# Kernel optimization log

Hardware: AMD Instinct MI355X
Metric: run time of the kernel (lower is better)

The kernel has to match this reference:

```python
import jax, jax.numpy as jnp
import numpy as np

# sym8 decomposition low-pass filter (pywt convention, 16 taps)
SYM8_DEC_LO = np.array([
    -0.0033824159510061256, -0.0005421323317911481, 0.03169508781149298,
    0.007607487324917605, -0.1432942383508097, -0.061273359067658524,
    0.4813596512583722, 0.7771857517005235, 0.3644418948353314,
    -0.05194583810770904, -0.027219029917056003, 0.049137179673607506,
    0.003808752013890615, -0.01495225833704823, -0.0003029205147213668,
    0.0018899503327594609], dtype=np.float64)

MAX_LEV = 8
POWER = 2.0
EPS = 1e-12


def _filters():
    dec_lo = jnp.asarray(SYM8_DEC_LO, dtype=jnp.float32)
    n = dec_lo.shape[0]
    alt = jnp.where(jnp.arange(n) % 2 == 0, 1.0, -1.0).astype(jnp.float32)
    dec_hi = alt * dec_lo[::-1]  # quadrature mirror filter
    # conv_general_dilated is cross-correlation (like torch conv1d in ptwt),
    # so flip the decomposition filters.
    return jnp.stack([dec_lo[::-1], dec_hi[::-1]])[:, None, :]  # [2,1,F] OIW


def _dwt_step(x, filt):
    # x: [N, L] -> [2N, L_out]; per node the (approx, detail) pair is interleaved,
    # which yields pywt 'natural' packet order after repeated application.
    F = filt.shape[-1]
    L = x.shape[1]
    padl = (2 * F - 3) // 2            # ptwt _fwt_pad, reflect mode
    padr = padl + (L % 2)              # extra right pad for odd lengths
    xp = jnp.pad(x, ((0, 0), (padl, padr)), mode='reflect')
    y = jax.lax.conv_general_dilated(
        xp[:, None, :], filt, window_strides=(2,), padding='VALID')  # [N,2,L']
    return y.reshape(-1, y.shape[-1])


def reference(pt_data):
    B = pt_data.shape[0]
    filt = _filters()
    x = pt_data
    for _ in range(MAX_LEV):           # fixed, small tree depth (8 levels)
        x = _dwt_step(x, filt)
    wp = x.reshape(B, 2 ** MAX_LEV, -1)         # [B, 256, L_final] natural order
    wp_log = jnp.log(jnp.abs(wp) ** POWER + EPS)
    # torch: stack(dim=-1) -> [B, L, P]; unsqueeze(1); permute(0,1,3,2) -> [B,1,P,L]
    return wp_log[:, None]             # [B, 1, 256, L_final]


def setup_inputs() -> dict:
    key = jax.random.key(0)
    pt_data = jax.random.normal(key, (128, 65536), dtype=jnp.float32)
    return {"pt_data": pt_data}
```

## Files before the change

kernel.cpp:

```cpp
#include <hip/hip_runtime.h>


#define BT 512

__device__ __constant__ float FL[16] = {
     0.0018899503327594609f, -0.0003029205147213668f, -0.01495225833704823f,
     0.003808752013890615f,   0.049137179673607506f,  -0.027219029917056003f,
    -0.05194583810770904f,    0.3644418948353314f,     0.7771857517005235f,
     0.4813596512583722f,    -0.061273359067658524f,  -0.1432942383508097f,
     0.007607487324917605f,   0.03169508781149298f,   -0.0005421323317911481f,
    -0.0033824159510061256f
};

__device__ __constant__ float FH[16] = {
     0.0033824159510061256f, -0.0005421323317911481f, -0.03169508781149298f,
     0.007607487324917605f,   0.1432942383508097f,    -0.061273359067658524f,
    -0.4813596512583722f,     0.7771857517005235f,    -0.3644418948353314f,
    -0.05194583810770904f,    0.027219029917056003f,   0.049137179673607506f,
    -0.003808752013890615f,  -0.01495225833704823f,    0.0003029205147213668f,
     0.0018899503327594609f
};

__device__ __constant__ float FLE[8] = {
     0.0018899503327594609f, -0.01495225833704823f,  0.049137179673607506f,
    -0.05194583810770904f,   0.7771857517005235f,   -0.061273359067658524f,
     0.007607487324917605f, -0.0005421323317911481f };
__device__ __constant__ float FLO[8] = {
    -0.0003029205147213668f, 0.003808752013890615f, -0.027219029917056003f,
     0.3644418948353314f,    0.4813596512583722f,   -0.1432942383508097f,
     0.03169508781149298f,  -0.0033824159510061256f };
__device__ __constant__ float FHE[8] = {
     0.0033824159510061256f, -0.03169508781149298f,  0.1432942383508097f,
    -0.4813596512583722f,   -0.3644418948353314f,    0.027219029917056003f,
    -0.003808752013890615f,  0.0003029205147213668f };
__device__ __constant__ float FHO[8] = {
    -0.0005421323317911481f, 0.007607487324917605f, -0.061273359067658524f,
     0.7771857517005235f,   -0.05194583810770904f,   0.049137179673607506f,
    -0.01495225833704823f,   0.0018899503327594609f };

__device__ __forceinline__ int reflect(int q, int L) {
    q = (q < 0) ? -q : q;
    return (q >= L) ? (2 * L - 2 - q) : q;
}

__device__ __forceinline__ void load20(const float* __restrict__ lds, int base,
                                       float w[20]) {
#pragma unroll
    for (int k = 0; k < 5; ++k) {
        const float4 v = *reinterpret_cast<const float4*>(&lds[base + 4 * k]);
        w[4 * k] = v.x; w[4 * k + 1] = v.y; w[4 * k + 2] = v.z; w[4 * k + 3] = v.w;
    }
}

__device__ __forceinline__ void conv2(const float w[20], float& lo0, float& hi0,
                                      float& lo1, float& hi1) {
    lo0 = hi0 = lo1 = hi1 = 0.f;
#pragma unroll
    for (int t = 0; t < 16; ++t) {
        const float cl = FL[t], ch = FH[t];
        lo0 = fmaf(w[t], cl, lo0);
        hi0 = fmaf(w[t], ch, hi0);
        lo1 = fmaf(w[t + 2], cl, lo1);
        hi1 = fmaf(w[t + 2], ch, hi1);
    }
}

template <int Pin, int Wout, int Sin, int Sout, int Lc>
__device__ __forceinline__ void f03_stage(const float* __restrict__ in,
                                          float* __restrict__ out, int o_lo) {
    constexpr int GPS = Wout / 2;
    for (int g = threadIdx.x; g < Pin * GPS; g += BT) {
        const int r = g / GPS;
        const int u = g - r * GPS;
        const int s0 = 2 * u;
        const int q0 = o_lo + s0;
        const float* pin = in + r * Sin;
        float lo0, hi0, lo1, hi1;
        if (q0 >= 0 && q0 + 2 <= Lc) {
            float w[20];
            load20(pin, 4 * u, w);
            conv2(w, lo0, hi0, lo1, hi1);
        } else {
#pragma unroll
            for (int e = 0; e < 2; ++e) {
                const int jr = reflect(q0 + e, Lc);
                const int rb = 2 * (jr - o_lo);
                float l = 0.f, h = 0.f;
#pragma unroll
                for (int t = 0; t < 16; ++t) {
                    const float v = pin[rb + t];
                    l = fmaf(v, FL[t], l);
                    h = fmaf(v, FH[t], h);
                }
                if (e == 0) { lo0 = l; hi0 = h; } else { lo1 = l; hi1 = h; }
            }
        }
        *reinterpret_cast<float2*>(&out[(2 * r) * Sout + s0])     = make_float2(lo0, lo1);
        *reinterpret_cast<float2*>(&out[(2 * r + 1) * Sout + s0]) = make_float2(hi0, hi1);
    }
}

__global__ __launch_bounds__(BT, 8) void dwt_f03(
    const float* __restrict__ x, float* __restrict__ y) {
    constexpr int M  = 258;
    constexpr int WX = 4338, SX = 4340;
    constexpr int W0 = 2162, S0 = 2164;
    constexpr int W1 = 1074, S1 = 1076;
    constexpr int W2 = 530,  S2 = 532;
    __shared__ __align__(16) float bufA[4340];
    __shared__ __align__(16) float bufB[4328];

    const int seg = blockIdx.x;
    const int n   = blockIdx.y;
    const int b0  = M * seg;
    const int a2  = 2 * b0 - 14;
    const int c1  = 4 * b0 - 42;
    const int a0  = 8 * b0 - 98;
    const int px0 = 16 * b0 - 210;
    const float* row = x + (size_t)n * 65536;

    if (px0 >= 0 && px0 + WX <= 65536) {
        const float2* rp = reinterpret_cast<const float2*>(row + px0);
        for (int h = threadIdx.x; h < WX / 2; h += BT)
            *reinterpret_cast<float2*>(&bufA[2 * h]) = rp[h];
    } else {
        for (int p = threadIdx.x; p < WX; p += BT)
            bufA[p] = row[reflect(px0 + p, 65536)];
    }
    __syncthreads();

    f03_stage<1, W0, SX, S0, 32775>(bufA, bufB, a0);
    __syncthreads();
    f03_stage<2, W1, S0, S1, 16395>(bufB, bufA, c1);
    __syncthreads();
    f03_stage<4, W2, S1, S2, 8205>(bufA, bufB, a2);
    __syncthreads();

    {
        constexpr int GPS = M / 2;
        float* yg = y + (size_t)(16 * n) * 4112;
        for (int g = threadIdx.x; g < 8 * GPS; g += BT) {
            const int r  = g / GPS;
            const int u  = g - r * GPS;
            const int j0 = b0 + 2 * u;
            if (j0 >= 4110) continue;
            float w[20];
            load20(bufB + r * S2, 4 * u, w);
            float lo0, hi0, lo1, hi1;
            conv2(w, lo0, hi0, lo1, hi1);
            float* y0 = yg + (size_t)(2 * r) * 4112 + j0;
            float* y1 = y0 + 4112;
            if (j0 + 1 < 4110) {
                *reinterpret_cast<float2*>(y0) = make_float2(lo0, lo1);
                *reinterpret_cast<float2*>(y1) = make_float2(hi0, hi1);
            } else {
                y0[0] = lo0; y1[0] = hi0;
            }
        }
    }
}

__device__ __forceinline__ void eo_put(float* __restrict__ E, float* __restrict__ O,
                                       int q, float v) {
    ((q & 1) ? O : E)[8 + (q >> 1)] = v;
}

__device__ __forceinline__ void read12(const float* __restrict__ b, int w0,
                                       float* __restrict__ r) {
#pragma unroll
    for (int k = 0; k < 3; ++k) {
        const float4 v = *reinterpret_cast<const float4*>(&b[w0 + 4 * k]);
        r[4 * k] = v.x; r[4 * k + 1] = v.y; r[4 * k + 2] = v.z; r[4 * k + 3] = v.w;
    }
}

template <int OFF>
__device__ __forceinline__ void conv4eo(const float e[12], const float o[12],
                                        float lo[4], float hi[4]) {
#pragma unroll
    for (int d = 0; d < 4; ++d) { lo[d] = 0.f; hi[d] = 0.f; }
#pragma unroll
    for (int s = 0; s < 8; ++s) {
        const float fle = FLE[s], flo = FLO[s], fhe = FHE[s], fho = FHO[s];
#pragma unroll
        for (int d = 0; d < 4; ++d) {
            const float ev = e[OFF + d + s], ov = o[OFF + d + s];
            lo[d] = fmaf(ev, fle, lo[d]);
            lo[d] = fmaf(ov, flo, lo[d]);
            hi[d] = fmaf(ev, fhe, hi[d]);
            hi[d] = fmaf(ov, fho, hi[d]);
        }
    }
}

template <int Ls, int P, int Sin, int Sout, bool LOG>
__device__ __forceinline__ void stage_eo(const float* __restrict__ inb,
                                         float* __restrict__ outb,
                                         float* __restrict__ outg) {
    constexpr int H    = Ls / 2;
    constexpr int LOUT = H + 7;
    constexpr int GPS  = (LOUT + 3) / 4;
    constexpr int SEi  = Sin / 2;
    constexpr int SEo  = Sout / 2;
    for (int g = threadIdx.x; g < P * GPS; g += BT) {
        const int p  = g / GPS;
        const int u  = g - p * GPS;
        const int j0 = 4 * u;
        const float* Ei = inb + p * Sin;
        const float* Oi = Ei + SEi;
        float e[12], o[12];
        read12(Ei, 4 * u, e);
        read12(Oi, 4 * u, o);
        float lo[4], hi[4];
        conv4eo<1>(e, o, lo, hi);
        if (LOG) {
            float r0[4], r1[4];
#pragma unroll
            for (int d = 0; d < 4; ++d) {
                r0[d] = __logf(fmaf(lo[d], lo[d], 1e-12f));
                r1[d] = __logf(fmaf(hi[d], hi[d], 1e-12f));
            }
            float* y0 = outg + (2 * p) * 270 + j0;
            float* y1 = y0 + 270;
            if (j0 + 3 < 270) {
                *reinterpret_cast<float2*>(y0)     = make_float2(r0[0], r0[1]);
                *reinterpret_cast<float2*>(y0 + 2) = make_float2(r0[2], r0[3]);
                *reinterpret_cast<float2*>(y1)     = make_float2(r1[0], r1[1]);
                *reinterpret_cast<float2*>(y1 + 2) = make_float2(r1[2], r1[3]);
            } else {
                *reinterpret_cast<float2*>(y0) = make_float2(r0[0], r0[1]);
                *reinterpret_cast<float2*>(y1) = make_float2(r1[0], r1[1]);
            }
        } else {
            float* El = outb + (2 * p) * Sout;
            float* Ol = El + SEo;
            float* Eh = outb + (2 * p + 1) * Sout;
            float* Oh = Eh + SEo;
            if (j0 + 3 < LOUT) {
                *reinterpret_cast<float2*>(&El[8 + 2 * u]) = make_float2(lo[0], lo[2]);
                *reinterpret_cast<float2*>(&Ol[8 + 2 * u]) = make_float2(lo[1], lo[3]);
                *reinterpret_cast<float2*>(&Eh[8 + 2 * u]) = make_float2(hi[0], hi[2]);
                *reinterpret_cast<float2*>(&Oh[8 + 2 * u]) = make_float2(hi[1], hi[3]);
            } else {
#pragma unroll
                for (int d = 0; d < 4; ++d)
                    if (j0 + d < LOUT) {
                        eo_put(El, Ol, j0 + d, lo[d]);
                        eo_put(Eh, Oh, j0 + d, hi[d]);
                    }
            }
            if (j0 <= 14 || j0 >= LOUT - 18) {
#pragma unroll
                for (int d = 0; d < 4; ++d) {
                    const int j = j0 + d;
                    if (j >= 1 && j <= 14) {
                        eo_put(El, Ol, -j, lo[d]);
                        eo_put(Eh, Oh, -j, hi[d]);
                    }
                    if (j >= LOUT - 15 && j <= LOUT - 2) {
                        eo_put(El, Ol, 2 * LOUT - 2 - j, lo[d]);
                        eo_put(Eh, Oh, 2 * LOUT - 2 - j, hi[d]);
                    }
                }
            }
        }
    }
}

__global__ __launch_bounds__(BT, 8) void dwt_quad_eo(
    const float* __restrict__ x, float* __restrict__ y) {
    __shared__ __align__(16) float bufA[4320];
    __shared__ __align__(16) float bufB[4544];

    const int m = blockIdx.x;
    const float* row = x + (size_t)m * 4112;
    float* Ex = bufA;
    float* Ox = bufA + 2076;
    for (int i = threadIdx.x; i < 2055; i += BT) {
        const float2 v = reinterpret_cast<const float2*>(row)[i];
        Ex[8 + i] = v.x;
        Ox[8 + i] = v.y;
        if (i >= 1 && i <= 7)       eo_put(Ex, Ox, -2 * i, v.x);
        if (i <= 6)                 eo_put(Ex, Ox, -(2 * i + 1), v.y);
        if (i >= 2048)              eo_put(Ex, Ox, 8218 - 2 * i, v.x);
        if (i >= 2047 && i <= 2053) eo_put(Ex, Ox, 8217 - 2 * i, v.y);
    }
    __syncthreads();
    stage_eo<4110, 1, 4152, 2104, false>(bufA, bufB, nullptr);
    __syncthreads();
    stage_eo<2062, 2, 2104, 1080, false>(bufB, bufA, nullptr);
    __syncthreads();
    stage_eo<1038, 4, 1080, 568, false>(bufA, bufB, nullptr);
    __syncthreads();
    stage_eo<526, 8, 568, 0, true>(bufB, nullptr, y + (size_t)m * 4320);
}

extern "C" void kernel_launch(void* const* d_in, const int* in_sizes, int n_in,
                              void* d_out, int out_size, void* d_ws, size_t ws_size,
                              hipStream_t stream) {
    const float* in = (const float*)d_in[0];
    float* out = (float*)d_out;
    float* wsB = (float*)d_ws;
    (void)ws_size; (void)out_size; (void)n_in; (void)in_sizes;

    { dim3 g(16, 128); dwt_f03<<<g, BT, 0, stream>>>(in, wsB); }
    dwt_quad_eo<<<2048, BT, 0, stream>>>(wsB, out);
}
```

Baseline: 74.02 us.

## Write intermediate in even/odd padded layout and load rows via direct global-to-LDS

The first kernel now writes its level-4 output straight into the padded even/odd split layout (including reflected halos) that the second kernel consumes, using a row stride of 4160. The second kernel can then copy each row into LDS with 16-byte direct global-to-LDS loads instead of deinterleaving and writing halos itself. Interior segments of the first kernel also use 4-byte global_load_lds for the input window. The aim is to cut VGPR round-trips and scatter work in the loads, at the cost of scattered strided global stores in the first kernel's epilogue and a slightly larger LDS buffer. The workspace layout changes, and the last 16-byte chunk reads a little past each logical row into padding.

```diff
diff --git a/kernel.cpp b/kernel.cpp
--- a/kernel.cpp
+++ b/kernel.cpp
@@ -11,7 +11,6 @@
      0.007607487324917605f,   0.03169508781149298f,   -0.0005421323317911481f,
     -0.0033824159510061256f
 };
-
 __device__ __constant__ float FH[16] = {
      0.0033824159510061256f, -0.0005421323317911481f, -0.03169508781149298f,
      0.007607487324917605f,   0.1432942383508097f,    -0.061273359067658524f,
@@ -20,7 +19,6 @@
     -0.003808752013890615f,  -0.01495225833704823f,    0.0003029205147213668f,
      0.0018899503327594609f
 };
-
 __device__ __constant__ float FLE[8] = {
      0.0018899503327594609f, -0.01495225833704823f,  0.049137179673607506f,
     -0.05194583810770904f,   0.7771857517005235f,   -0.061273359067658524f,
@@ -43,6 +41,17 @@
     return (q >= L) ? (2 * L - 2 - q) : q;
 }
 
+__device__ __forceinline__ void gload_lds16(const float* g, float* l) {
+    __builtin_amdgcn_global_load_lds(
+        (const __attribute__((address_space(1))) void*)g,
+        (__attribute__((address_space(3))) void*)l, 16, 0, 0);
+}
+__device__ __forceinline__ void gload_lds4(const float* g, float* l) {
+    __builtin_amdgcn_global_load_lds(
+        (const __attribute__((address_space(1))) void*)g,
+        (__attribute__((address_space(3))) void*)l, 4, 0, 0);
+}
+
 __device__ __forceinline__ void load20(const float* __restrict__ lds, int base,
                                        float w[20]) {
 #pragma unroll
@@ -63,6 +72,11 @@
         lo1 = fmaf(w[t + 2], cl, lo1);
         hi1 = fmaf(w[t + 2], ch, hi1);
     }
+}
+
+__device__ __forceinline__ void eo_put(float* __restrict__ E, float* __restrict__ O,
+                                       int q, float v) {
+    ((q & 1) ? O : E)[8 + (q >> 1)] = v;
 }
 
 template <int Pin, int Wout, int Sin, int Sout, int Lc>
@@ -107,7 +121,7 @@
     constexpr int W0 = 2162, S0 = 2164;
     constexpr int W1 = 1074, S1 = 1076;
     constexpr int W2 = 530,  S2 = 532;
-    __shared__ __align__(16) float bufA[4340];
+    __shared__ __align__(16) float bufA[4352];
     __shared__ __align__(16) float bufB[4328];
 
     const int seg = blockIdx.x;
@@ -119,10 +133,11 @@
     const int px0 = 16 * b0 - 210;
     const float* row = x + (size_t)n * 65536;
 
-    if (px0 >= 0 && px0 + WX <= 65536) {
-        const float2* rp = reinterpret_cast<const float2*>(row + px0);
-        for (int h = threadIdx.x; h < WX / 2; h += BT)
-            *reinterpret_cast<float2*>(&bufA[2 * h]) = rp[h];
+    if (seg >= 1 && seg <= 14) {
+        const int wave = threadIdx.x >> 6;
+        const int lane = threadIdx.x & 63;
+        for (int c = wave; c < 68; c += 8)
+            gload_lds4(row + px0 + c * 64 + lane, &bufA[c * 64]);
     } else {
         for (int p = threadIdx.x; p < WX; p += BT)
             bufA[p] = row[reflect(px0 + p, 65536)];
@@ -138,7 +153,7 @@
 
     {
         constexpr int GPS = M / 2;
-        float* yg = y + (size_t)(16 * n) * 4112;
+        float* yg = y + (size_t)(16 * n) * 4160;
         for (int g = threadIdx.x; g < 8 * GPS; g += BT) {
             const int r  = g / GPS;
             const int u  = g - r * GPS;
@@ -148,21 +163,30 @@
             load20(bufB + r * S2, 4 * u, w);
             float lo0, hi0, lo1, hi1;
             conv2(w, lo0, hi0, lo1, hi1);
-            float* y0 = yg + (size_t)(2 * r) * 4112 + j0;
-            float* y1 = y0 + 4112;
-            if (j0 + 1 < 4110) {
-                *reinterpret_cast<float2*>(y0) = make_float2(lo0, lo1);
-                *reinterpret_cast<float2*>(y1) = make_float2(hi0, hi1);
-            } else {
-                y0[0] = lo0; y1[0] = hi0;
+            float* Elo = yg + (size_t)(2 * r) * 4160;
+            float* Olo = Elo + 2076;
+            float* Ehi = Elo + 4160;
+            float* Ohi = Ehi + 2076;
+            const int s = 8 + (j0 >> 1);
+            Elo[s] = lo0; Olo[s] = lo1; Ehi[s] = hi0; Ohi[s] = hi1;
+            if (j0 <= 14 || j0 >= 4094) {
+#pragma unroll
+                for (int e = 0; e < 2; ++e) {
+                    const int j = j0 + e;
+                    const float vl = e ? lo1 : lo0;
+                    const float vh = e ? hi1 : hi0;
+                    if (j >= 1 && j <= 14) {
+                        eo_put(Elo, Olo, -j, vl);
+                        eo_put(Ehi, Ohi, -j, vh);
+                    }
+                    if (j >= 4095 && j <= 4108) {
+                        eo_put(Elo, Olo, 8218 - j, vl);
+                        eo_put(Ehi, Ohi, 8218 - j, vh);
+                    }
+                }
             }
         }
     }
-}
-
-__device__ __forceinline__ void eo_put(float* __restrict__ E, float* __restrict__ O,
-                                       int q, float v) {
-    ((q & 1) ? O : E)[8 + (q >> 1)] = v;
 }
 
 __device__ __forceinline__ void read12(const float* __restrict__ b, int w0,
@@ -269,23 +293,18 @@
 
 __global__ __launch_bounds__(BT, 8) void dwt_quad_eo(
     const float* __restrict__ x, float* __restrict__ y) {
-    __shared__ __align__(16) float bufA[4320];
+    __shared__ __align__(16) float bufA[4352];
     __shared__ __align__(16) float bufB[4544];
 
     const int m = blockIdx.x;
-    const float* row = x + (size_t)m * 4112;
-    float* Ex = bufA;
-    float* Ox = bufA + 2076;
-    for (int i = threadIdx.x; i < 2055; i += BT) {
-        const float2 v = reinterpret_cast<const float2*>(row)[i];
-        Ex[8 + i] = v.x;
-        Ox[8 + i] = v.y;
-        if (i >= 1 && i <= 7)       eo_put(Ex, Ox, -2 * i, v.x);
-        if (i <= 6)                 eo_put(Ex, Ox, -(2 * i + 1), v.y);
-        if (i >= 2048)              eo_put(Ex, Ox, 8218 - 2 * i, v.x);
-        if (i >= 2047 && i <= 2053) eo_put(Ex, Ox, 8217 - 2 * i, v.y);
-    }
-    __syncthreads();
+    const float* row = x + (size_t)m * 4160;
+
+    const int wave = threadIdx.x >> 6;
+    const int lane = threadIdx.x & 63;
+    for (int c = wave; c < 17; c += 8)
+        gload_lds16(row + c * 256 + lane * 4, &bufA[c * 256]);
+    __syncthreads();
+
     stage_eo<4110, 1, 4152, 2104, false>(bufA, bufB, nullptr);
     __syncthreads();
     stage_eo<2062, 2, 2104, 1080, false>(bufB, bufA, nullptr);
```

New measurement: 76.63 us. 1.04x slower.

## Write intermediate in even/odd split layout and bulk-load via global_load_lds

Applied to the files above, without the earlier changes.

The first kernel now writes its level-4 output directly in the even/odd deinterleaved padded layout that the second kernel consumes, using a wider 4160-float row stride. The second kernel then fills shared memory with direct global-to-LDS 16-byte loads instead of per-thread float2 loads plus scatter. Only a small fixup pass remains, writing the reflect-padding halos. The aim is to remove the deinterleave work and register round-trips on the input side. In exchange the producer's stores become scalar and strided rather than float2 vectors.

```diff
diff --git a/kernel.cpp b/kernel.cpp
--- a/kernel.cpp
+++ b/kernel.cpp
@@ -11,7 +11,6 @@
      0.007607487324917605f,   0.03169508781149298f,   -0.0005421323317911481f,
     -0.0033824159510061256f
 };
-
 __device__ __constant__ float FH[16] = {
      0.0033824159510061256f, -0.0005421323317911481f, -0.03169508781149298f,
      0.007607487324917605f,   0.1432942383508097f,    -0.061273359067658524f,
@@ -20,7 +19,6 @@
     -0.003808752013890615f,  -0.01495225833704823f,    0.0003029205147213668f,
      0.0018899503327594609f
 };
-
 __device__ __constant__ float FLE[8] = {
      0.0018899503327594609f, -0.01495225833704823f,  0.049137179673607506f,
     -0.05194583810770904f,   0.7771857517005235f,   -0.061273359067658524f,
@@ -43,6 +41,12 @@
     return (q >= L) ? (2 * L - 2 - q) : q;
 }
 
+__device__ __forceinline__ void gload_lds16(const float* g, float* l) {
+    __builtin_amdgcn_global_load_lds(
+        (const __attribute__((address_space(1))) void*)g,
+        (__attribute__((address_space(3))) void*)l, 16, 0, 0);
+}
+
 __device__ __forceinline__ void load20(const float* __restrict__ lds, int base,
                                        float w[20]) {
 #pragma unroll
@@ -63,6 +67,11 @@
         lo1 = fmaf(w[t + 2], cl, lo1);
         hi1 = fmaf(w[t + 2], ch, hi1);
     }
+}
+
+__device__ __forceinline__ void eo_put(float* __restrict__ E, float* __restrict__ O,
+                                       int q, float v) {
+    ((q & 1) ? O : E)[8 + (q >> 1)] = v;
 }
 
 template <int Pin, int Wout, int Sin, int Sout, int Lc>
@@ -138,7 +147,7 @@
 
     {
         constexpr int GPS = M / 2;
-        float* yg = y + (size_t)(16 * n) * 4112;
+        float* yg = y + (size_t)(16 * n) * 4160;
         for (int g = threadIdx.x; g < 8 * GPS; g += BT) {
             const int r  = g / GPS;
             const int u  = g - r * GPS;
@@ -148,21 +157,14 @@
             load20(bufB + r * S2, 4 * u, w);
             float lo0, hi0, lo1, hi1;
             conv2(w, lo0, hi0, lo1, hi1);
-            float* y0 = yg + (size_t)(2 * r) * 4112 + j0;
-            float* y1 = y0 + 4112;
-            if (j0 + 1 < 4110) {
-                *reinterpret_cast<float2*>(y0) = make_float2(lo0, lo1);
-                *reinterpret_cast<float2*>(y1) = make_float2(hi0, hi1);
-            } else {
-                y0[0] = lo0; y1[0] = hi0;
-            }
+            float* Elo = yg + (size_t)(2 * r) * 4160;
+            const int s = 8 + (j0 >> 1);
+            Elo[s]          = lo0;
+            Elo[2076 + s]   = lo1;
+            Elo[4160 + s]   = hi0;
+            Elo[6236 + s]   = hi1;
         }
     }
-}
-
-__device__ __forceinline__ void eo_put(float* __restrict__ E, float* __restrict__ O,
-                                       int q, float v) {
-    ((q & 1) ? O : E)[8 + (q >> 1)] = v;
 }
 
 __device__ __forceinline__ void read12(const float* __restrict__ b, int w0,
@@ -269,23 +271,29 @@
 
 __global__ __launch_bounds__(BT, 8) void dwt_quad_eo(
     const float* __restrict__ x, float* __restrict__ y) {
-    __shared__ __align__(16) float bufA[4320];
+    __shared__ __align__(16) float bufA[4352];
     __shared__ __align__(16) float bufB[4544];
 
     const int m = blockIdx.x;
-    const float* row = x + (size_t)m * 4112;
-    float* Ex = bufA;
-    float* Ox = bufA + 2076;
-    for (int i = threadIdx.x; i < 2055; i += BT) {
-        const float2 v = reinterpret_cast<const float2*>(row)[i];
-        Ex[8 + i] = v.x;
-        Ox[8 + i] = v.y;
-        if (i >= 1 && i <= 7)       eo_put(Ex, Ox, -2 * i, v.x);
-        if (i <= 6)                 eo_put(Ex, Ox, -(2 * i + 1), v.y);
-        if (i >= 2048)              eo_put(Ex, Ox, 8218 - 2 * i, v.x);
-        if (i >= 2047 && i <= 2053) eo_put(Ex, Ox, 8217 - 2 * i, v.y);
-    }
-    __syncthreads();
+    const float* row = x + (size_t)m * 4160;
+
+    const int wave = threadIdx.x >> 6;
+    const int lane = threadIdx.x & 63;
+    for (int c = wave; c < 17; c += 8)
+        gload_lds16(row + c * 256 + lane * 4, &bufA[c * 256]);
+    __syncthreads();
+
+    if (threadIdx.x < 28) {
+        const int t = threadIdx.x;
+        float* Ex = bufA;
+        float* Ox = bufA + 2076;
+        if (t < 7)       Ex[7 - t]          = Ex[9 + t];
+        else if (t < 14) Ox[14 - t]         = Ox[t + 1];
+        else if (t < 21) Ex[2063 + (t - 14)] = Ex[2062 - (t - 14)];
+        else             Ox[2063 + (t - 21)] = Ox[2061 - (t - 21)];
+    }
+    __syncthreads();
+
     stage_eo<4110, 1, 4152, 2104, false>(bufA, bufB, nullptr);
     __syncthreads();
     stage_eo<2062, 2, 2104, 1080, false>(bufB, bufA, nullptr);
```

After: 76.72 us. 3.6% more time.
